# Kernel optimization log

Hardware: AMD Instinct MI355X
Metric: run time of the kernel (lower is better)

Reference implementation:

```python
import jax, jax.numpy as jnp
import numpy as np

N = 16384
D_IN = 512
HEADS = 2
D_HEAD = 256
EPS_LN = 1e-5
NEG_SLOPE = 0.2


def l2norm_dim0(x):
    # F.normalize(x, p=2, dim=0): per-column L2 normalization
    n = jnp.sqrt(jnp.sum(x * x, axis=0, keepdims=True))
    return x / jnp.maximum(n, 1e-12)


def layer_norm(x, g, b):
    m = jnp.mean(x, axis=-1, keepdims=True)
    v = jnp.mean((x - m) ** 2, axis=-1, keepdims=True)
    return (x - m) * jax.lax.rsqrt(v + EPS_LN) * g + b


def gat_conv(x, edge_index, W, att_src, att_dst, bias):
    # PyG GATConv with add_self_loops=True, concat=True, negative_slope=0.2
    n = x.shape[0]
    loops = jnp.arange(n, dtype=edge_index.dtype)
    src = jnp.concatenate([edge_index[0], loops])
    dst = jnp.concatenate([edge_index[1], loops])
    h = (x @ W).reshape(n, HEADS, D_HEAD)            # [N, H, Dh]
    a_src = jnp.sum(h * att_src, axis=-1)            # [N, H]
    a_dst = jnp.sum(h * att_dst, axis=-1)            # [N, H]
    e = a_src[src] + a_dst[dst]                      # [E, H]
    e = jnp.where(e >= 0, e, NEG_SLOPE * e)          # leaky_relu
    # segment softmax over incoming edges of each dst node
    emax = jax.ops.segment_max(e, dst, num_segments=n)
    ex = jnp.exp(e - emax[dst])
    den = jax.ops.segment_sum(ex, dst, num_segments=n)
    alpha = ex / den[dst]                            # [E, H]
    msg = h[src] * alpha[:, :, None]                 # [E, H, Dh]
    out = jax.ops.segment_sum(msg, dst, num_segments=n)  # [N, H, Dh]
    return out.reshape(n, HEADS * D_HEAD) + bias


def setup_inputs() -> dict:
    key = jax.random.key(0)
    ks = jax.random.split(key, 16)
    def glorot(k, shape):
        lim = np.sqrt(6.0 / (shape[0] + shape[-1]))
        return jax.random.uniform(k, shape, jnp.float32, -lim, lim)
    x = jax.random.normal(ks[0], (N, D_IN), jnp.float32)
    edge_index = jax.random.randint(ks[1], (2, 524288), 0, N, jnp.int64)
    return {
        "x": x,
        "edge_index": edge_index,
        "W": glorot(ks[2], (D_IN, HEADS * D_HEAD)),
        "att_src": glorot(ks[3], (HEADS, D_HEAD)),
        "att_dst": glorot(ks[4], (HEADS, D_HEAD)),
        "bias_conv": jnp.zeros((HEADS * D_HEAD,), jnp.float32),
        "Wa": glorot(ks[5], (512, 256)), "ba": jnp.zeros((256,), jnp.float32),
        "ga": jnp.ones((256,), jnp.float32), "bga": jnp.zeros((256,), jnp.float32),
        "W1": glorot(ks[6], (256, 128)), "b1": jnp.zeros((128,), jnp.float32),
        "g1": jnp.ones((128,), jnp.float32), "bg1": jnp.zeros((128,), jnp.float32),
        "W2": glorot(ks[7], (128, 64)), "b2": jnp.zeros((64,), jnp.float32),
        "g2": jnp.ones((64,), jnp.float32), "bg2": jnp.zeros((64,), jnp.float32),
        "W3": glorot(ks[8], (64, 3)), "b3": jnp.zeros((3,), jnp.float32),
    }


def reference(x, edge_index, W, att_src, att_dst, bias_conv,
              Wa, ba, ga, bga, W1, b1, g1, bg1,
              W2, b2, g2, bg2, W3, b3):
    h = l2norm_dim0(x)
    h = gat_conv(h, edge_index, W, att_src, att_dst, bias_conv)
    h = jax.nn.relu(h)
    h = l2norm_dim0(h)
    h = layer_norm(h @ Wa + ba, ga, bga)
    h = jax.nn.relu(h)
    h = l2norm_dim0(h)
    h = layer_norm(h @ W1 + b1, g1, bg1)
    h = jax.nn.relu(h)
    h = l2norm_dim0(h)
    h = layer_norm(h @ W2 + b2, g2, bg2)
    h = jax.nn.relu(h)
    h = l2norm_dim0(h)
    h = h @ W3 + b3                                  # [N, 3]
    # torch.cdist(h, h, p=2)
    sq = jnp.sum(h * h, axis=-1)
    d2 = sq[:, None] + sq[None, :] - 2.0 * (h @ h.T)
    return jnp.sqrt(jnp.maximum(d2, 0.0))
```

## Files before the change

kernel.cpp:

```cpp
#include <hip/hip_runtime.h>
#include <math.h>


typedef __bf16 bf16x8 __attribute__((ext_vector_type(8)));
typedef __bf16 bf16x4 __attribute__((ext_vector_type(4)));
typedef __bf16 bf16x2 __attribute__((ext_vector_type(2)));
typedef float  f32x4  __attribute__((ext_vector_type(4)));
typedef short  short8 __attribute__((ext_vector_type(8)));

static __device__ __forceinline__ float leaky02(float e){ return e >= 0.f ? e : 0.2f*e; }

static __device__ __forceinline__ float wred_sum(float v){
  #pragma unroll
  for (int m = 1; m < 64; m <<= 1) v += __shfl_xor(v, m);
  return v;
}
static __device__ __forceinline__ float wred_max(float v){
  #pragma unroll
  for (int m = 1; m < 64; m <<= 1) v = fmaxf(v, __shfl_xor(v, m));
  return v;
}

__global__ void colnorm_sq(const float* __restrict__ X, float* __restrict__ ss, int R, int C){
  int c = blockIdx.x*blockDim.x + threadIdx.x;
  if (c >= C) return;
  int r0 = blockIdx.y * 128;
  int r1 = r0 + 128; if (r1 > R) r1 = R;
  float s = 0.f;
  for (int r = r0; r < r1; ++r){ float v = X[(size_t)r*C + c]; s = fmaf(v, v, s); }
  atomicAdd(&ss[c], s);
}

__global__ void colnorm_sq_hl(const __bf16* __restrict__ H, const __bf16* __restrict__ L,
                              float* __restrict__ ss, int R, int C){
  int c = blockIdx.x*blockDim.x + threadIdx.x;
  if (c >= C) return;
  int r0 = blockIdx.y * 128;
  int r1 = r0 + 128; if (r1 > R) r1 = R;
  float s = 0.f;
  for (int r = r0; r < r1; ++r){
    float v = (float)H[(size_t)r*C + c] + (float)L[(size_t)r*C + c];
    s = fmaf(v, v, s);
  }
  atomicAdd(&ss[c], s);
}

__global__ __launch_bounds__(256) void split_tr_scaled(const float* __restrict__ B,
    const float* __restrict__ ss,
    __bf16* __restrict__ TH, __bf16* __restrict__ TL, int K, int N){
  __shared__ float tile[32][33];
  int lx = threadIdx.x & 31, ly = threadIdx.x >> 5;
  int kb = blockIdx.y*32, nb = blockIdx.x*32;
  #pragma unroll
  for (int i = 0; i < 4; i++){
    int kr = kb + ly + i*8;
    float inv = 1.f / fmaxf(sqrtf(ss[kr]), 1e-12f);
    tile[ly + i*8][lx] = B[(size_t)kr*N + nb + lx] * inv;
  }
  __syncthreads();
  #pragma unroll
  for (int i = 0; i < 4; i++){
    int nl = ly + i*8;
    float v = tile[lx][nl];
    __bf16 h = (__bf16)v;
    TH[(size_t)(nb + nl)*K + kb + lx] = h;
    TL[(size_t)(nb + nl)*K + kb + lx] = (__bf16)(v - (float)h);
  }
}

__global__ __launch_bounds__(256) void gemm_bf16x3(
    const __bf16* __restrict__ Ah, const __bf16* __restrict__ Al,
    const __bf16* __restrict__ Bth, const __bf16* __restrict__ Btl,
    float* __restrict__ C, int M, int N, int K)
{
  __shared__ __align__(16) __bf16 sAh[128][40];
  __shared__ __align__(16) __bf16 sAl[128][40];
  __shared__ __align__(16) __bf16 sBh[64][40];
  __shared__ __align__(16) __bf16 sBl[64][40];
  int tid = threadIdx.x;
  int lane = tid & 63, wave = tid >> 6;
  int wr = wave >> 1, wc = wave & 1;
  int rowBase = blockIdx.x << 7, colBase = blockIdx.y << 6;

  int ar = tid >> 2;
  int ac = tid & 3;

  short8 rAh0, rAh1, rAl0, rAl1, rBh, rBl;
  auto loadA = [&](int k0){
    rAh0 = *(const short8*)(Ah + (size_t)(rowBase + ar     )*K + k0 + ac*8);
    rAh1 = *(const short8*)(Ah + (size_t)(rowBase + ar + 64)*K + k0 + ac*8);
    rAl0 = *(const short8*)(Al + (size_t)(rowBase + ar     )*K + k0 + ac*8);
    rAl1 = *(const short8*)(Al + (size_t)(rowBase + ar + 64)*K + k0 + ac*8);
    rBh  = *(const short8*)(Bth + (size_t)(colBase + ar)*K + k0 + ac*8);
    rBl  = *(const short8*)(Btl + (size_t)(colBase + ar)*K + k0 + ac*8);
  };

  f32x4 acc[4][2];
  #pragma unroll
  for (int m = 0; m < 4; m++)
    #pragma unroll
    for (int n = 0; n < 2; n++) acc[m][n] = (f32x4){0.f,0.f,0.f,0.f};

  loadA(0);
  int nsteps = K >> 5;
  for (int s = 0; s < nsteps; ++s){
    __syncthreads();
    *(short8*)&sAh[ar][ac*8]      = rAh0;
    *(short8*)&sAh[ar+64][ac*8]   = rAh1;
    *(short8*)&sAl[ar][ac*8]      = rAl0;
    *(short8*)&sAl[ar+64][ac*8]   = rAl1;
    *(short8*)&sBh[ar][ac*8]      = rBh;
    *(short8*)&sBl[ar][ac*8]      = rBl;
    if (s + 1 < nsteps) loadA((s+1) << 5);
    __syncthreads();

    int kslot = lane >> 4;
    bf16x8 fah[4], fal[4], fbh[2], fbl[2];
    #pragma unroll
    for (int m = 0; m < 4; m++){
      int r = wr*64 + m*16 + (lane & 15);
      fah[m] = *(const bf16x8*)&sAh[r][kslot*8];
      fal[m] = *(const bf16x8*)&sAl[r][kslot*8];
    }
    #pragma unroll
    for (int n = 0; n < 2; n++){
      int c = wc*32 + n*16 + (lane & 15);
      fbh[n] = *(const bf16x8*)&sBh[c][kslot*8];
      fbl[n] = *(const bf16x8*)&sBl[c][kslot*8];
    }
    #pragma unroll
    for (int m = 0; m < 4; m++)
      #pragma unroll
      for (int n = 0; n < 2; n++){
        acc[m][n] = __builtin_amdgcn_mfma_f32_16x16x32_bf16(fah[m], fbh[n], acc[m][n], 0,0,0);
        acc[m][n] = __builtin_amdgcn_mfma_f32_16x16x32_bf16(fah[m], fbl[n], acc[m][n], 0,0,0);
        acc[m][n] = __builtin_amdgcn_mfma_f32_16x16x32_bf16(fal[m], fbh[n], acc[m][n], 0,0,0);
      }
  }

  int rg = lane >> 4, cl = lane & 15;
  #pragma unroll
  for (int m = 0; m < 4; m++)
    #pragma unroll
    for (int n = 0; n < 2; n++)
      #pragma unroll
      for (int j = 0; j < 4; j++)
        C[(size_t)(rowBase + wr*64 + m*16 + rg*4 + j)*N + colBase + wc*32 + n*16 + cl] = acc[m][n][j];
}

__global__ __launch_bounds__(256) void gemm_f32a_bf16x3(
    const float* __restrict__ A,
    const __bf16* __restrict__ Bth, const __bf16* __restrict__ Btl,
    float* __restrict__ C, int M, int N, int K)
{
  __shared__ __align__(16) __bf16 sAh[128][40];
  __shared__ __align__(16) __bf16 sAl[128][40];
  __shared__ __align__(16) __bf16 sBh[64][40];
  __shared__ __align__(16) __bf16 sBl[64][40];
  int tid = threadIdx.x;
  int lane = tid & 63, wave = tid >> 6;
  int wr = wave >> 1, wc = wave & 1;
  int rowBase = blockIdx.x << 7, colBase = blockIdx.y << 6;

  int ar = tid >> 2;
  int ac = tid & 3;

  float4 rA0a, rA0b, rA1a, rA1b; short8 rBh, rBl;
  auto loadA = [&](int k0){
    const float* p0 = A + (size_t)(rowBase + ar)*K + k0 + ac*8;
    rA0a = *(const float4*)p0; rA0b = *(const float4*)(p0 + 4);
    const float* p1 = A + (size_t)(rowBase + ar + 64)*K + k0 + ac*8;
    rA1a = *(const float4*)p1; rA1b = *(const float4*)(p1 + 4);
    rBh  = *(const short8*)(Bth + (size_t)(colBase + ar)*K + k0 + ac*8);
    rBl  = *(const short8*)(Btl + (size_t)(colBase + ar)*K + k0 + ac*8);
  };
  auto splitst = [&](float4 a, float4 b, __bf16* dh, __bf16* dl){
    float t[8] = {a.x,a.y,a.z,a.w,b.x,b.y,b.z,b.w};
    bf16x8 hv, lv;
    #pragma unroll
    for (int j = 0; j < 8; j++){
      __bf16 h = (__bf16)t[j]; hv[j] = h; lv[j] = (__bf16)(t[j] - (float)h);
    }
    *(bf16x8*)dh = hv; *(bf16x8*)dl = lv;
  };

  f32x4 acc[4][2];
  #pragma unroll
  for (int m = 0; m < 4; m++)
    #pragma unroll
    for (int n = 0; n < 2; n++) acc[m][n] = (f32x4){0.f,0.f,0.f,0.f};

  loadA(0);
  int nsteps = K >> 5;
  for (int s = 0; s < nsteps; ++s){
    __syncthreads();
    splitst(rA0a, rA0b, &sAh[ar][ac*8],    &sAl[ar][ac*8]);
    splitst(rA1a, rA1b, &sAh[ar+64][ac*8], &sAl[ar+64][ac*8]);
    *(short8*)&sBh[ar][ac*8] = rBh;
    *(short8*)&sBl[ar][ac*8] = rBl;
    if (s + 1 < nsteps) loadA((s+1) << 5);
    __syncthreads();

    int kslot = lane >> 4;
    bf16x8 fah[4], fal[4], fbh[2], fbl[2];
    #pragma unroll
    for (int m = 0; m < 4; m++){
      int r = wr*64 + m*16 + (lane & 15);
      fah[m] = *(const bf16x8*)&sAh[r][kslot*8];
      fal[m] = *(const bf16x8*)&sAl[r][kslot*8];
    }
    #pragma unroll
    for (int n = 0; n < 2; n++){
      int c = wc*32 + n*16 + (lane & 15);
      fbh[n] = *(const bf16x8*)&sBh[c][kslot*8];
      fbl[n] = *(const bf16x8*)&sBl[c][kslot*8];
    }
    #pragma unroll
    for (int m = 0; m < 4; m++)
      #pragma unroll
      for (int n = 0; n < 2; n++){
        acc[m][n] = __builtin_amdgcn_mfma_f32_16x16x32_bf16(fah[m], fbh[n], acc[m][n], 0,0,0);
        acc[m][n] = __builtin_amdgcn_mfma_f32_16x16x32_bf16(fah[m], fbl[n], acc[m][n], 0,0,0);
        acc[m][n] = __builtin_amdgcn_mfma_f32_16x16x32_bf16(fal[m], fbh[n], acc[m][n], 0,0,0);
      }
  }

  int rg = lane >> 4, cl = lane & 15;
  #pragma unroll
  for (int m = 0; m < 4; m++)
    #pragma unroll
    for (int n = 0; n < 2; n++)
      #pragma unroll
      for (int j = 0; j < 4; j++)
        C[(size_t)(rowBase + wr*64 + m*16 + rg*4 + j)*N + colBase + wc*32 + n*16 + cl] = acc[m][n][j];
}

__global__ __launch_bounds__(256) void att_deg_kernel(const float* __restrict__ h,
    const float* __restrict__ att_src, const float* __restrict__ att_dst,
    float* __restrict__ asrc, float* __restrict__ adst,
    const int* __restrict__ dst, int* __restrict__ deg, int nAttBlk, int E){
  if ((int)blockIdx.x < nAttBlk){
    int lane = threadIdx.x & 63;
    int node = blockIdx.x*4 + (threadIdx.x >> 6);
    const float4* hp = (const float4*)(h + (size_t)node*512);
    float4 v0 = hp[lane], v1 = hp[64 + lane];
    float4 as0 = ((const float4*)att_src)[lane], as1 = ((const float4*)att_src)[64+lane];
    float4 ad0 = ((const float4*)att_dst)[lane], ad1 = ((const float4*)att_dst)[64+lane];
    float s0 = v0.x*as0.x + v0.y*as0.y + v0.z*as0.z + v0.w*as0.w;
    float s1 = v1.x*as1.x + v1.y*as1.y + v1.z*as1.z + v1.w*as1.w;
    float d0 = v0.x*ad0.x + v0.y*ad0.y + v0.z*ad0.z + v0.w*ad0.w;
    float d1 = v1.x*ad1.x + v1.y*ad1.y + v1.z*ad1.z + v1.w*ad1.w;
    s0 = wred_sum(s0); s1 = wred_sum(s1); d0 = wred_sum(d0); d1 = wred_sum(d1);
    if (lane == 0){
      asrc[2*node] = s0; asrc[2*node+1] = s1;
      adst[2*node] = d0; adst[2*node+1] = d1;
    }
  } else {
    int e = (blockIdx.x - nAttBlk)*256 + threadIdx.x;
    if (e < E) atomicAdd(&deg[dst[e]], 1);
  }
}

__global__ __launch_bounds__(1024) void scan_kernel(const int* __restrict__ deg,
    int* __restrict__ offs, int* __restrict__ cursor, int n){
  __shared__ int part[1024];
  int t = threadIdx.x;
  int chunk = (n + 1023) >> 10;
  int base = t * chunk;
  int loc[32];
  int local = 0;
  for (int k = 0; k < chunk; k++){
    int idx = base + k; loc[k] = local;
    if (idx < n) local += deg[idx] + 1;
  }
  part[t] = local; __syncthreads();
  for (int off = 1; off < 1024; off <<= 1){
    int v = (t >= off) ? part[t-off] : 0; __syncthreads();
    part[t] += v; __syncthreads();
  }
  int excl = part[t] - local;
  for (int k = 0; k < chunk; k++){
    int idx = base + k;
    if (idx < n){ int o = excl + loc[k]; offs[idx] = o; cursor[idx] = o; }
  }
  if (t == 1023) offs[n] = part[1023];
}
__global__ void scatter_edges(const int* __restrict__ src, const int* __restrict__ dst,
                              int* cursor, int* __restrict__ ssrc, int E, int N){
  int e = blockIdx.x*blockDim.x + threadIdx.x;
  if (e < E){
    int d = dst[e]; int pos = atomicAdd(&cursor[d], 1); ssrc[pos] = src[e];
  } else if (e < E + N){
    int i = e - E; int pos = atomicAdd(&cursor[i], 1); ssrc[pos] = i;
  }
}

__global__ __launch_bounds__(256) void gat_aggregate_w(const float* __restrict__ h,
    const int* __restrict__ offs, const int* __restrict__ ssrc,
    const float* __restrict__ asrc, const float* __restrict__ adst,
    const float* __restrict__ bias,
    __bf16* __restrict__ H, __bf16* __restrict__ L, int N){
  int lane = threadIdx.x & 63;
  int d = blockIdx.x*4 + (threadIdx.x >> 6);
  int beg = offs[d], end = offs[d+1], cnt = end - beg;
  float ad0 = adst[2*d], ad1 = adst[2*d+1];

  int dbase = lane*8;
  bool head0 = dbase < 256;
  f32x4 acc0 = {0.f,0.f,0.f,0.f}, acc1 = {0.f,0.f,0.f,0.f};

  if (cnt <= 64){
    int sreg = 0; float le0 = -1e30f, le1 = -1e30f;
    if (lane < cnt){
      sreg = ssrc[beg + lane];
      float2 a = *(const float2*)&asrc[2*sreg];
      le0 = leaky02(a.x + ad0); le1 = leaky02(a.y + ad1);
    }
    float m0 = wred_max(le0), m1 = wred_max(le1);
    float e0 = (lane < cnt) ? __expf(le0 - m0) : 0.f;
    float e1 = (lane < cnt) ? __expf(le1 - m1) : 0.f;
    float inv0 = 1.f / wred_sum(e0), inv1 = 1.f / wred_sum(e1);
    float al0 = e0*inv0, al1 = e1*inv1;
    for (int o = 0; o < cnt; ++o){
      int s = __shfl(sreg, o);
      float aA = __shfl(al0, o), aB = __shfl(al1, o);
      float al = head0 ? aA : aB;
      const float4* hp = (const float4*)&h[(size_t)s*512 + dbase];
      float4 v0 = hp[0], v1 = hp[1];
      acc0[0] = fmaf(al, v0.x, acc0[0]); acc0[1] = fmaf(al, v0.y, acc0[1]);
      acc0[2] = fmaf(al, v0.z, acc0[2]); acc0[3] = fmaf(al, v0.w, acc0[3]);
      acc1[0] = fmaf(al, v1.x, acc1[0]); acc1[1] = fmaf(al, v1.y, acc1[1]);
      acc1[2] = fmaf(al, v1.z, acc1[2]); acc1[3] = fmaf(al, v1.w, acc1[3]);
    }
  } else {
    float m0 = -1e30f, m1 = -1e30f;
    for (int o = beg + lane; o < end; o += 64){
      int s = ssrc[o]; float2 a = *(const float2*)&asrc[2*s];
      m0 = fmaxf(m0, leaky02(a.x + ad0)); m1 = fmaxf(m1, leaky02(a.y + ad1));
    }
    m0 = wred_max(m0); m1 = wred_max(m1);
    float q0 = 0.f, q1 = 0.f;
    for (int o = beg + lane; o < end; o += 64){
      int s = ssrc[o]; float2 a = *(const float2*)&asrc[2*s];
      q0 += __expf(leaky02(a.x + ad0) - m0); q1 += __expf(leaky02(a.y + ad1) - m1);
    }
    float inv0 = 1.f / wred_sum(q0), inv1 = 1.f / wred_sum(q1);
    for (int c0 = beg; c0 < end; c0 += 64){
      int cc = end - c0; if (cc > 64) cc = 64;
      int sreg = 0; float al0 = 0.f, al1 = 0.f;
      if (lane < cc){
        sreg = ssrc[c0 + lane];
        float2 a = *(const float2*)&asrc[2*sreg];
        al0 = __expf(leaky02(a.x + ad0) - m0) * inv0;
        al1 = __expf(leaky02(a.y + ad1) - m1) * inv1;
      }
      for (int o = 0; o < cc; ++o){
        int s = __shfl(sreg, o);
        float aA = __shfl(al0, o), aB = __shfl(al1, o);
        float al = head0 ? aA : aB;
        const float4* hp = (const float4*)&h[(size_t)s*512 + dbase];
        float4 v0 = hp[0], v1 = hp[1];
        acc0[0] = fmaf(al, v0.x, acc0[0]); acc0[1] = fmaf(al, v0.y, acc0[1]);
        acc0[2] = fmaf(al, v0.z, acc0[2]); acc0[3] = fmaf(al, v0.w, acc0[3]);
        acc1[0] = fmaf(al, v1.x, acc1[0]); acc1[1] = fmaf(al, v1.y, acc1[1]);
        acc1[2] = fmaf(al, v1.z, acc1[2]); acc1[3] = fmaf(al, v1.w, acc1[3]);
      }
    }
  }

  float4 bi0 = *(const float4*)&bias[dbase];
  float4 bi1 = *(const float4*)&bias[dbase + 4];
  float o_[8];
  o_[0] = fmaxf(acc0[0] + bi0.x, 0.f); o_[1] = fmaxf(acc0[1] + bi0.y, 0.f);
  o_[2] = fmaxf(acc0[2] + bi0.z, 0.f); o_[3] = fmaxf(acc0[3] + bi0.w, 0.f);
  o_[4] = fmaxf(acc1[0] + bi1.x, 0.f); o_[5] = fmaxf(acc1[1] + bi1.y, 0.f);
  o_[6] = fmaxf(acc1[2] + bi1.z, 0.f); o_[7] = fmaxf(acc1[3] + bi1.w, 0.f);
  bf16x8 hv, lv;
  #pragma unroll
  for (int j = 0; j < 8; j++){
    __bf16 hh = (__bf16)o_[j]; hv[j] = hh; lv[j] = (__bf16)(o_[j] - (float)hh);
  }
  *(bf16x8*)&H[(size_t)d*512 + dbase] = hv;
  *(bf16x8*)&L[(size_t)d*512 + dbase] = lv;
}

template<int C, bool SPLIT>
__global__ __launch_bounds__(256) void ln_relu_t(float* __restrict__ Z,
    const float* __restrict__ bias, const float* __restrict__ g,
    const float* __restrict__ bg, __bf16* __restrict__ H, __bf16* __restrict__ L, int R){
  constexpr int VW = C / 64;
  int lane = threadIdx.x & 63, wid = threadIdx.x >> 6;
  int r = blockIdx.x*4 + wid;
  size_t base = (size_t)r*C + lane*VW;
  float v[VW], bi[VW], gm[VW], bt[VW];
  if constexpr (VW == 4){
    float4 t0 = *(const float4*)&Z[base];
    float4 t1 = *(const float4*)&bias[lane*4];
    float4 t2 = *(const float4*)&g[lane*4];
    float4 t3 = *(const float4*)&bg[lane*4];
    v[0]=t0.x; v[1]=t0.y; v[2]=t0.z; v[3]=t0.w;
    bi[0]=t1.x; bi[1]=t1.y; bi[2]=t1.z; bi[3]=t1.w;
    gm[0]=t2.x; gm[1]=t2.y; gm[2]=t2.z; gm[3]=t2.w;
    bt[0]=t3.x; bt[1]=t3.y; bt[2]=t3.z; bt[3]=t3.w;
  } else if constexpr (VW == 2){
    float2 t0 = *(const float2*)&Z[base];
    float2 t1 = *(const float2*)&bias[lane*2];
    float2 t2 = *(const float2*)&g[lane*2];
    float2 t3 = *(const float2*)&bg[lane*2];
    v[0]=t0.x; v[1]=t0.y; bi[0]=t1.x; bi[1]=t1.y;
    gm[0]=t2.x; gm[1]=t2.y; bt[0]=t3.x; bt[1]=t3.y;
  } else {
    v[0] = Z[base]; bi[0] = bias[lane]; gm[0] = g[lane]; bt[0] = bg[lane];
  }
  float sum = 0.f;
  #pragma unroll
  for (int j = 0; j < VW; j++){ v[j] += bi[j]; sum += v[j]; }
  sum = wred_sum(sum);
  float mean = sum * (1.f/C);
  float sq = 0.f;
  #pragma unroll
  for (int j = 0; j < VW; j++){ float dz = v[j]-mean; sq += dz*dz; }
  sq = wred_sum(sq);
  float rs = 1.f / sqrtf(sq*(1.f/C) + 1e-5f);
  float o[VW];
  #pragma unroll
  for (int j = 0; j < VW; j++) o[j] = fmaxf((v[j]-mean)*rs*gm[j] + bt[j], 0.f);
  if constexpr (VW == 4) *(float4*)&Z[base] = make_float4(o[0],o[1],o[2],o[3]);
  else if constexpr (VW == 2) *(float2*)&Z[base] = make_float2(o[0],o[1]);
  else Z[base] = o[0];
  if constexpr (SPLIT){
    if constexpr (VW == 4){
      bf16x4 hv, lv;
      #pragma unroll
      for (int j = 0; j < 4; j++){ hv[j] = (__bf16)o[j]; lv[j] = (__bf16)(o[j]-(float)hv[j]); }
      *(bf16x4*)&H[base] = hv; *(bf16x4*)&L[base] = lv;
    } else if constexpr (VW == 2){
      bf16x2 hv, lv;
      #pragma unroll
      for (int j = 0; j < 2; j++){ hv[j] = (__bf16)o[j]; lv[j] = (__bf16)(o[j]-(float)hv[j]); }
      *(bf16x2*)&H[base] = hv; *(bf16x2*)&L[base] = lv;
    } else {
      __bf16 hv = (__bf16)o[0];
      H[base] = hv; L[base] = (__bf16)(o[0]-(float)hv);
    }
  }
}

__global__ __launch_bounds__(256) void gemm64_ln(const float* __restrict__ A,
    const float* __restrict__ W2, const float* __restrict__ ss,
    const float* __restrict__ b2, const float* __restrict__ g2,
    const float* __restrict__ bg2, float* __restrict__ Zout, int N){
  __shared__ float w2s[128*64];
  __shared__ float invs[128];
  __shared__ float rowbuf[4][128];
  int t = threadIdx.x;
  int lane = t & 63, wid = t >> 6;
  if (t < 128) invs[t] = 1.f / fmaxf(sqrtf(ss[t]), 1e-12f);
  __syncthreads();
  #pragma unroll
  for (int i = 0; i < 32; i++){
    int idx = t + i*256;
    w2s[idx] = W2[idx] * invs[idx >> 6];
  }
  int r = blockIdx.x*4 + wid;
  float2 rv = *(const float2*)&A[(size_t)r*128 + lane*2];
  rowbuf[wid][lane*2]   = rv.x;
  rowbuf[wid][lane*2+1] = rv.y;
  __syncthreads();
  float acc = b2[lane];
  #pragma unroll 8
  for (int k = 0; k < 128; ++k)
    acc = fmaf(rowbuf[wid][k], w2s[k*64 + lane], acc);
  float mean = wred_sum(acc) * (1.f/64.f);
  float dz = acc - mean;
  float var = wred_sum(dz*dz) * (1.f/64.f);
  float rs = 1.f / sqrtf(var + 1e-5f);
  float o = fmaxf(dz*rs*g2[lane] + bg2[lane], 0.f);
  Zout[(size_t)r*64 + lane] = o;
}

__global__ __launch_bounds__(256) void final_hf4(const float* __restrict__ A,
    const float* __restrict__ W3, const float* __restrict__ ss,
    const float* __restrict__ b3, float4* __restrict__ hf4, int N){
  __shared__ float w[64*3];
  __shared__ float b[3];
  if (threadIdx.x < 192){
    int k = threadIdx.x / 3;
    w[threadIdx.x] = W3[threadIdx.x] / fmaxf(sqrtf(ss[k]), 1e-12f);
  }
  if (threadIdx.x < 3) b[threadIdx.x] = b3[threadIdx.x];
  __syncthreads();
  int r = blockIdx.x*blockDim.x + threadIdx.x;
  if (r >= N) return;
  float x = b[0], y = b[1], z = b[2];
  #pragma unroll 8
  for (int k = 0; k < 64; ++k){
    float a = A[(size_t)r*64 + k];
    x = fmaf(a, w[k*3],   x);
    y = fmaf(a, w[k*3+1], y);
    z = fmaf(a, w[k*3+2], z);
  }
  float sq = x*x + y*y + z*z;
  hf4[r] = make_float4(x, y, z, sq);
}

__global__ __launch_bounds__(256) void cdist_kernel(const float4* __restrict__ hf,
                                                    float* __restrict__ out, int N){
  int i0 = blockIdx.y * 8;
  int j0 = (blockIdx.x*256 + threadIdx.x)*4;
  float4 a[8];
  #pragma unroll
  for (int q = 0; q < 8; q++) a[q] = hf[i0 + q];
  float4 b0 = hf[j0], b1 = hf[j0+1], b2 = hf[j0+2], b3 = hf[j0+3];
  #pragma unroll
  for (int q = 0; q < 8; q++){
    f32x4 r; float d;
    d = a[q].w + b0.w - 2.f*(a[q].x*b0.x + a[q].y*b0.y + a[q].z*b0.z); r[0] = sqrtf(fmaxf(d, 0.f));
    d = a[q].w + b1.w - 2.f*(a[q].x*b1.x + a[q].y*b1.y + a[q].z*b1.z); r[1] = sqrtf(fmaxf(d, 0.f));
    d = a[q].w + b2.w - 2.f*(a[q].x*b2.x + a[q].y*b2.y + a[q].z*b2.z); r[2] = sqrtf(fmaxf(d, 0.f));
    d = a[q].w + b3.w - 2.f*(a[q].x*b3.x + a[q].y*b3.y + a[q].z*b3.z); r[3] = sqrtf(fmaxf(d, 0.f));
    __builtin_nontemporal_store(r, (f32x4*)&out[(size_t)(i0 + q)*N + j0]);
  }
}

extern "C" void kernel_launch(void* const* d_in, const int* in_sizes, int n_in,
                              void* d_out, int out_size, void* d_ws, size_t ws_size,
                              hipStream_t stream){
  const int N = in_sizes[0] / 512;
  const int E = in_sizes[1] / 2;

  const float* x         = (const float*)d_in[0];
  const int*   ei        = (const int*)  d_in[1];
  const float* W         = (const float*)d_in[2];
  const float* att_src   = (const float*)d_in[3];
  const float* att_dst   = (const float*)d_in[4];
  const float* bias_conv = (const float*)d_in[5];
  const float* Wa  = (const float*)d_in[6];
  const float* ba  = (const float*)d_in[7];
  const float* ga  = (const float*)d_in[8];
  const float* bga = (const float*)d_in[9];
  const float* W1  = (const float*)d_in[10];
  const float* b1  = (const float*)d_in[11];
  const float* g1  = (const float*)d_in[12];
  const float* bg1 = (const float*)d_in[13];
  const float* W2  = (const float*)d_in[14];
  const float* b2  = (const float*)d_in[15];
  const float* g2  = (const float*)d_in[16];
  const float* bg2 = (const float*)d_in[17];
  const float* W3  = (const float*)d_in[18];
  const float* b3  = (const float*)d_in[19];

  const int* e_src = ei;
  const int* e_dst = ei + E;

  size_t off = 0;
  auto alloc = [&](size_t bytes)->char*{
    size_t o = off; off += (bytes + 255) & ~(size_t)255;
    return (char*)d_ws + o;
  };
  float* bufA  = (float*)alloc((size_t)N*512*4);
  float* bufB  = (float*)alloc((size_t)N*512*4);
  __bf16* Ah   = (__bf16*)alloc((size_t)N*512*2);
  __bf16* Al   = (__bf16*)alloc((size_t)N*512*2);
  __bf16* Bth  = (__bf16*)alloc(512*512*2);
  __bf16* Btl  = (__bf16*)alloc(512*512*2);
  char* zbase  = alloc(5*512*4 + (size_t)N*4);
  float* ss1 = (float*)zbase;
  float* ss2 = ss1 + 512;
  float* ss3 = ss2 + 512;
  float* ss4 = ss3 + 512;
  float* ss5 = ss4 + 512;
  int*   deg = (int*)(ss5 + 512);
  float* asrc  = (float*)alloc((size_t)N*2*4);
  float* adst  = (float*)alloc((size_t)N*2*4);
  float4* hf4  = (float4*)alloc((size_t)N*16);
  int* offs    = (int*)alloc((size_t)(N+1)*4);
  int* cursor  = (int*)alloc((size_t)N*4);
  int* ssrc    = (int*)alloc((size_t)(E+N)*4);

  float* outF = (float*)d_out;

  hipMemsetAsync(zbase, 0, 5*512*4 + (size_t)N*4, stream);

  colnorm_sq<<<dim3(2,128), 256, 0, stream>>>(x, ss1, N, 512);
  split_tr_scaled<<<dim3(16,16), 256, 0, stream>>>(W, ss1, Bth, Btl, 512, 512);
  gemm_f32a_bf16x3<<<dim3(N/128, 8), 256, 0, stream>>>(x, Bth, Btl, bufA, N, 512, 512);

  int nAttBlk = N/4;
  att_deg_kernel<<<nAttBlk + (E+255)/256, 256, 0, stream>>>(bufA, att_src, att_dst,
                                                            asrc, adst, e_dst, deg, nAttBlk, E);
  scan_kernel<<<1, 1024, 0, stream>>>(deg, offs, cursor, N);
  scatter_edges<<<(E+N+255)/256, 256, 0, stream>>>(e_src, e_dst, cursor, ssrc, E, N);
  gat_aggregate_w<<<N/4, 256, 0, stream>>>(bufA, offs, ssrc, asrc, adst, bias_conv,
                                           Ah, Al, N);

  colnorm_sq_hl<<<dim3(2,128), 256, 0, stream>>>(Ah, Al, ss2, N, 512);
  split_tr_scaled<<<dim3(8,16), 256, 0, stream>>>(Wa, ss2, Bth, Btl, 512, 256);
  gemm_bf16x3<<<dim3(N/128, 4), 256, 0, stream>>>(Ah, Al, Bth, Btl, bufB, N, 256, 512);
  ln_relu_t<256,true><<<N/4, 256, 0, stream>>>(bufB, ba, ga, bga, Ah, Al, N);

  colnorm_sq<<<dim3(1,128), 256, 0, stream>>>(bufB, ss3, N, 256);
  split_tr_scaled<<<dim3(4,8), 256, 0, stream>>>(W1, ss3, Bth, Btl, 256, 128);
  gemm_bf16x3<<<dim3(N/128, 2), 256, 0, stream>>>(Ah, Al, Bth, Btl, bufA, N, 128, 256);
  ln_relu_t<128,false><<<N/4, 256, 0, stream>>>(bufA, b1, g1, bg1,
                                                (__bf16*)nullptr, (__bf16*)nullptr, N);

  colnorm_sq<<<dim3(1,128), 256, 0, stream>>>(bufA, ss4, N, 128);
  gemm64_ln<<<N/4, 256, 0, stream>>>(bufA, W2, ss4, b2, g2, bg2, bufB, N);

  colnorm_sq<<<dim3(1,128), 256, 0, stream>>>(bufB, ss5, N, 64);
  final_hf4<<<(N+255)/256, 256, 0, stream>>>(bufB, W3, ss5, b3, hf4, N);
  cdist_kernel<<<dim3(N/1024, N/8), 256, 0, stream>>>(hf4, outF, N);
}
```

Baseline: 683.5 us.

## Fuse degree count into GEMM launch, merge scatter with attention, enlarge cdist tile

Degree counting now runs as extra blocks appended to the first GEMM's 1D grid, which lets the edge scatter be merged into the attention-logit kernel. That removes one kernel launch and lets independent graph work overlap with the dense work. Separately, the cdist kernel now computes 16 rows per block instead of 8, halving its grid height and reusing each column load across more rows, at the cost of more registers. The GEMM grid mapping changes from 2D to 1D and assumes M/128 is a power of two.

```diff
diff --git a/kernel.cpp b/kernel.cpp
--- a/kernel.cpp
+++ b/kernel.cpp
@@ -148,19 +148,28 @@
         C[(size_t)(rowBase + wr*64 + m*16 + rg*4 + j)*N + colBase + wc*32 + n*16 + cl] = acc[m][n][j];
 }
 
-__global__ __launch_bounds__(256) void gemm_f32a_bf16x3(
+__global__ __launch_bounds__(256) void gemm_f32a_bf16x3_deg(
     const float* __restrict__ A,
     const __bf16* __restrict__ Bth, const __bf16* __restrict__ Btl,
-    float* __restrict__ C, int M, int N, int K)
+    float* __restrict__ C,
+    const int* __restrict__ dst, int* __restrict__ deg,
+    int M, int N, int K, int nGemmBlk, int E)
 {
   __shared__ __align__(16) __bf16 sAh[128][40];
   __shared__ __align__(16) __bf16 sAl[128][40];
   __shared__ __align__(16) __bf16 sBh[64][40];
   __shared__ __align__(16) __bf16 sBl[64][40];
+  if ((int)blockIdx.x >= nGemmBlk){
+    int e = ((int)blockIdx.x - nGemmBlk)*256 + threadIdx.x;
+    if (e < E) atomicAdd(&deg[dst[e]], 1);
+    return;
+  }
+  int MB = M >> 7;
+  int rowBase = ((int)blockIdx.x & (MB-1)) << 7;
+  int colBase = ((int)blockIdx.x / MB) << 6;
   int tid = threadIdx.x;
   int lane = tid & 63, wave = tid >> 6;
   int wr = wave >> 1, wc = wave & 1;
-  int rowBase = blockIdx.x << 7, colBase = blockIdx.y << 6;
 
   int ar = tid >> 2;
   int ac = tid & 3;
@@ -235,10 +244,12 @@
         C[(size_t)(rowBase + wr*64 + m*16 + rg*4 + j)*N + colBase + wc*32 + n*16 + cl] = acc[m][n][j];
 }
 
-__global__ __launch_bounds__(256) void att_deg_kernel(const float* __restrict__ h,
+__global__ __launch_bounds__(256) void att_scatter_kernel(const float* __restrict__ h,
     const float* __restrict__ att_src, const float* __restrict__ att_dst,
     float* __restrict__ asrc, float* __restrict__ adst,
-    const int* __restrict__ dst, int* __restrict__ deg, int nAttBlk, int E){
+    const int* __restrict__ src, const int* __restrict__ dst,
+    int* __restrict__ cursor, int* __restrict__ ssrc,
+    int nAttBlk, int E, int N){
   if ((int)blockIdx.x < nAttBlk){
     int lane = threadIdx.x & 63;
     int node = blockIdx.x*4 + (threadIdx.x >> 6);
@@ -256,8 +267,12 @@
       adst[2*node] = d0; adst[2*node+1] = d1;
     }
   } else {
-    int e = (blockIdx.x - nAttBlk)*256 + threadIdx.x;
-    if (e < E) atomicAdd(&deg[dst[e]], 1);
+    int e = ((int)blockIdx.x - nAttBlk)*256 + threadIdx.x;
+    if (e < E){
+      int d = dst[e]; int pos = atomicAdd(&cursor[d], 1); ssrc[pos] = src[e];
+    } else if (e < E + N){
+      int i = e - E; int pos = atomicAdd(&cursor[i], 1); ssrc[pos] = i;
+    }
   }
 }
 
@@ -284,15 +299,6 @@
     if (idx < n){ int o = excl + loc[k]; offs[idx] = o; cursor[idx] = o; }
   }
   if (t == 1023) offs[n] = part[1023];
-}
-__global__ void scatter_edges(const int* __restrict__ src, const int* __restrict__ dst,
-                              int* cursor, int* __restrict__ ssrc, int E, int N){
-  int e = blockIdx.x*blockDim.x + threadIdx.x;
-  if (e < E){
-    int d = dst[e]; int pos = atomicAdd(&cursor[d], 1); ssrc[pos] = src[e];
-  } else if (e < E + N){
-    int i = e - E; int pos = atomicAdd(&cursor[i], 1); ssrc[pos] = i;
-  }
 }
 
 __global__ __launch_bounds__(256) void gat_aggregate_w(const float* __restrict__ h,
@@ -506,14 +512,14 @@
 
 __global__ __launch_bounds__(256) void cdist_kernel(const float4* __restrict__ hf,
                                                     float* __restrict__ out, int N){
-  int i0 = blockIdx.y * 8;
+  int i0 = blockIdx.y * 16;
   int j0 = (blockIdx.x*256 + threadIdx.x)*4;
-  float4 a[8];
-  #pragma unroll
-  for (int q = 0; q < 8; q++) a[q] = hf[i0 + q];
+  float4 a[16];
+  #pragma unroll
+  for (int q = 0; q < 16; q++) a[q] = hf[i0 + q];
   float4 b0 = hf[j0], b1 = hf[j0+1], b2 = hf[j0+2], b3 = hf[j0+3];
   #pragma unroll
-  for (int q = 0; q < 8; q++){
+  for (int q = 0; q < 16; q++){
     f32x4 r; float d;
     d = a[q].w + b0.w - 2.f*(a[q].x*b0.x + a[q].y*b0.y + a[q].z*b0.z); r[0] = sqrtf(fmaxf(d, 0.f));
     d = a[q].w + b1.w - 2.f*(a[q].x*b1.x + a[q].y*b1.y + a[q].z*b1.z); r[1] = sqrtf(fmaxf(d, 0.f));
@@ -584,13 +590,16 @@
 
   colnorm_sq<<<dim3(2,128), 256, 0, stream>>>(x, ss1, N, 512);
   split_tr_scaled<<<dim3(16,16), 256, 0, stream>>>(W, ss1, Bth, Btl, 512, 512);
-  gemm_f32a_bf16x3<<<dim3(N/128, 8), 256, 0, stream>>>(x, Bth, Btl, bufA, N, 512, 512);
-
+  int nGemmBlk = (N/128) * 8;
+  int nDegBlk  = (E + 255) / 256;
+  gemm_f32a_bf16x3_deg<<<nGemmBlk + nDegBlk, 256, 0, stream>>>(
+      x, Bth, Btl, bufA, e_dst, deg, N, 512, 512, nGemmBlk, E);
+
+  scan_kernel<<<1, 1024, 0, stream>>>(deg, offs, cursor, N);
   int nAttBlk = N/4;
-  att_deg_kernel<<<nAttBlk + (E+255)/256, 256, 0, stream>>>(bufA, att_src, att_dst,
-                                                            asrc, adst, e_dst, deg, nAttBlk, E);
-  scan_kernel<<<1, 1024, 0, stream>>>(deg, offs, cursor, N);
-  scatter_edges<<<(E+N+255)/256, 256, 0, stream>>>(e_src, e_dst, cursor, ssrc, E, N);
+  int nScatBlk = (E + N + 255) / 256;
+  att_scatter_kernel<<<nAttBlk + nScatBlk, 256, 0, stream>>>(
+      bufA, att_src, att_dst, asrc, adst, e_src, e_dst, cursor, ssrc, nAttBlk, E, N);
   gat_aggregate_w<<<N/4, 256, 0, stream>>>(bufA, offs, ssrc, asrc, adst, bias_conv,
                                            Ah, Al, N);
 
@@ -610,5 +619,5 @@
 
   colnorm_sq<<<dim3(1,128), 256, 0, stream>>>(bufB, ss5, N, 64);
   final_hf4<<<(N+255)/256, 256, 0, stream>>>(bufB, W3, ss5, b3, hf4, N);
-  cdist_kernel<<<dim3(N/1024, N/8), 256, 0, stream>>>(hf4, outF, N);
-}
+  cdist_kernel<<<dim3(N/1024, N/16), 256, 0, stream>>>(hf4, outF, N);
+}
```

Measured after the change: 689.3 us. No clear change (+0.8%).
